# Kernel optimization log

Hardware: AMD Instinct MI355X
Metric: run time of the kernel (lower is better)

## Reference

```python
import jax, jax.numpy as jnp
import numpy as np

B, T, C = 4, 2048, 1024
NH = 16
HD = C // NH  # 64

def setup_inputs() -> dict:
    key = jax.random.key(0)
    k1, k2, k3 = jax.random.split(key, 3)
    x = jax.random.normal(k1, (B, T, C), dtype=jnp.float32)
    w_qkv = jax.random.normal(k2, (C, 3 * C), dtype=jnp.float32) * (1.0 / np.sqrt(C))
    w_out = jax.random.normal(k3, (C, C), dtype=jnp.float32) * (1.0 / np.sqrt(C))
    b_out = jnp.zeros((C,), dtype=jnp.float32)
    return {"x": x, "w_qkv": w_qkv, "w_out": w_out, "b_out": b_out}

def reference(x, w_qkv, w_out, b_out):
    b, t, c = x.shape
    nh, hd = NH, c // NH
    qkv = x @ w_qkv                      # [b, t, 3c]
    q, k, v = jnp.split(qkv, 3, axis=-1)
    # [b, t, c] -> [b, nh, t, hd]
    def heads(z):
        return z.reshape(b, t, nh, hd).transpose(0, 2, 1, 3)
    q, k, v = heads(q), heads(k), heads(v)
    scale = 1.0 / jnp.sqrt(jnp.asarray(hd, dtype=x.dtype))
    scores = jnp.einsum('bhqd,bhkd->bhqk', q, k) * scale  # [b, nh, t, t]
    causal = jnp.tril(jnp.ones((t, t), dtype=bool))
    scores = jnp.where(causal, scores, jnp.asarray(-jnp.inf, dtype=scores.dtype))
    attn = jax.nn.softmax(scores, axis=-1)
    ctx = jnp.einsum('bhqk,bhkd->bhqd', attn, v)           # [b, nh, t, hd]
    ctx = ctx.transpose(0, 2, 1, 3).reshape(b, t, c)
    return ctx @ w_out + b_out
```

## Files before the change

### kernel.cpp

```cpp
#include <hip/hip_runtime.h>
#include <cmath>


typedef __bf16 bf16x4 __attribute__((ext_vector_type(4)));
typedef __bf16 bf16x8 __attribute__((ext_vector_type(8)));
typedef float  f32x4  __attribute__((ext_vector_type(4)));
typedef float  f32x16 __attribute__((ext_vector_type(16)));

__device__ __forceinline__ void gload_lds16(const __bf16* g, __bf16* l) {
    __builtin_amdgcn_global_load_lds(
        (const __attribute__((address_space(1))) void*)g,
        (__attribute__((address_space(3))) void*)l,
        16, 0, 0);
}

__device__ __forceinline__ unsigned packbf(float a, float b) {
    union { __bf16 h[2]; unsigned u; } t;
    t.h[0] = (__bf16)a; t.h[1] = (__bf16)b;
    return t.u;
}

__device__ __forceinline__ void permswap(unsigned& a, unsigned& b) {
    asm volatile("v_permlane32_swap_b32 %0, %1" : "+v"(a), "+v"(b));
}

#define BAR()  __builtin_amdgcn_s_barrier()
#define VM2()  { asm volatile("s_waitcnt vmcnt(2)" ::: "memory"); \
                 __builtin_amdgcn_sched_barrier(0); }

__global__ __launch_bounds__(256) void cast_bf16(const float* __restrict__ in,
                                                 __bf16* __restrict__ out, int n4) {
    int i = blockIdx.x * 256 + threadIdx.x;
    if (i >= n4) return;
    float4 f = *(const float4*)(in + (size_t)i * 4);
    bf16x4 o;
    o[0] = (__bf16)f.x; o[1] = (__bf16)f.y; o[2] = (__bf16)f.z; o[3] = (__bf16)f.w;
    *(bf16x4*)(out + (size_t)i * 4) = o;
}

__global__ __launch_bounds__(256) void transpose_cast(const float* __restrict__ W,
                                                      __bf16* __restrict__ WT,
                                                      int K, int N) {
    __shared__ float tile[32][33];
    const int n0 = blockIdx.x * 32, k0 = blockIdx.y * 32;
    const int tx = threadIdx.x & 31, ty = threadIdx.x >> 5;
    #pragma unroll
    for (int i = 0; i < 4; ++i)
        tile[ty + 8 * i][tx] = W[(size_t)(k0 + ty + 8 * i) * N + n0 + tx];
    __syncthreads();
    #pragma unroll
    for (int i = 0; i < 4; ++i)
        WT[(size_t)(n0 + ty + 8 * i) * K + k0 + tx] = (__bf16)tile[tx][ty + 8 * i];
}

__global__ __launch_bounds__(256) void transpose_v(const __bf16* __restrict__ qkv,
                                                   __bf16* __restrict__ Vt) {
    constexpr int T = 2048, R3C = 3072;
    __shared__ __bf16 tile[64][72];
    const int bh = blockIdx.y;
    const int b  = bh >> 4, h = bh & 15;
    const int kt = blockIdx.x * 64;
    const int tid = threadIdx.x;
    #pragma unroll
    for (int i = 0; i < 2; ++i) {
        int idx = tid + 256 * i;
        int kr  = idx >> 3;
        int c8  = idx & 7;
        *(uint4*)&tile[kr][c8 * 8] =
            *(const uint4*)(qkv + (size_t)(b * T + kt + kr) * R3C + 2048 + h * 64 + c8 * 8);
    }
    __syncthreads();
    #pragma unroll
    for (int i = 0; i < 2; ++i) {
        int idx = tid + 256 * i;
        int d   = idx >> 3;
        int k8  = idx & 7;
        union { __bf16 v[8]; uint4 u; } t;
        #pragma unroll
        for (int j = 0; j < 8; ++j) t.v[j] = tile[k8 * 8 + j][d];
        *(uint4*)(Vt + ((size_t)bh * 64 + d) * T + kt + k8 * 8) = t.u;
    }
}

__global__ __launch_bounds__(512) void gemm256(const __bf16* __restrict__ A,
                                               const __bf16* __restrict__ BT,
                                               __bf16* __restrict__ Cc,
                                               int M, int N, int K) {
    __shared__ __attribute__((aligned(16))) char lds[131072];
    const int tid = threadIdx.x, lane = tid & 63, w = tid >> 6;
    const int wr = w >> 2, wc = w & 3, cc = lane & 15, gg = lane >> 4;

    const int cpx = gridDim.x >> 3;
    const int swz = ((int)blockIdx.x & 7) * cpx + ((int)blockIdx.x >> 3);
    const int nbx = N >> 8;
    const int rowBase = (swz / nbx) << 8;
    const int colBase = (swz % nbx) << 8;
    const int NT = K >> 6;

    const int sChunk = (lane & 7) ^ (((lane >> 5) & 1) << 1);
    const int rsub   = lane >> 3;

    auto stA = [&](int t, int h) {
        const int buf = t & 1, k0 = (t % NT) * 64;
        #pragma unroll
        for (int l = 0; l < 2; ++l) {
            int idx   = l * 8 + w;
            int rbase = ((idx >> 3) << 7) + h * 64 + ((idx & 7) << 3);
            gload_lds16(A + (size_t)(rowBase + rbase + rsub) * K + k0 + sChunk * 8,
                        (__bf16*)(lds + buf * 65536 + rbase * 128 + lane * 16));
        }
    };
    auto stB = [&](int t, int h) {
        const int buf = t & 1, k0 = (t % NT) * 64;
        #pragma unroll
        for (int l = 0; l < 2; ++l) {
            int idx   = l * 8 + w;
            int rbase = ((idx >> 2) << 6) + h * 32 + ((idx & 3) << 3);
            gload_lds16(BT + (size_t)(colBase + rbase + rsub) * K + k0 + sChunk * 8,
                        (__bf16*)(lds + buf * 65536 + 32768 + rbase * 128 + lane * 16));
        }
    };

    f32x4 acc[8][4];
    #pragma unroll
    for (int i = 0; i < 8; ++i)
        #pragma unroll
        for (int j = 0; j < 4; ++j) acc[i][j] = f32x4{0.f, 0.f, 0.f, 0.f};
    bf16x8 afr[8], bfr[8];

    auto rdA = [&](int buf, int mh) {
        const char* base = lds + buf * 65536;
        #pragma unroll
        for (int i = 0; i < 4; ++i)
            #pragma unroll
            for (int kk = 0; kk < 2; ++kk) {
                int r  = wr * 128 + mh * 64 + i * 16 + cc;
                int cb = (kk * 64 + gg * 16) ^ (((cc >> 2) & 1) << 5);
                afr[i * 2 + kk] = *(const bf16x8*)(base + r * 128 + cb);
            }
    };
    auto rdB = [&](int buf) {
        const char* base = lds + buf * 65536 + 32768;
        #pragma unroll
        for (int j = 0; j < 4; ++j)
            #pragma unroll
            for (int kk = 0; kk < 2; ++kk) {
                int r  = wc * 64 + j * 16 + cc;
                int cb = (kk * 64 + gg * 16) ^ (((cc >> 2) & 1) << 5);
                bfr[j * 2 + kk] = *(const bf16x8*)(base + r * 128 + cb);
            }
    };

#define QMFMA(MH, NH)                                                        \
    _Pragma("unroll") for (int i = 0; i < 4; ++i)                            \
    _Pragma("unroll") for (int j = 0; j < 2; ++j)                            \
    _Pragma("unroll") for (int kk = 0; kk < 2; ++kk)                         \
        acc[(MH)*4 + i][(NH)*2 + j] = __builtin_amdgcn_mfma_f32_16x16x32_bf16( \
            afr[i*2 + kk], bfr[((NH)*2 + j)*2 + kk], acc[(MH)*4 + i][(NH)*2 + j], 0, 0, 0);

    stA(0, 0); stB(0, 0); stA(0, 1); stB(0, 1); stA(1, 0);
    VM2(); BAR();

    for (int t = 0; t < NT; ++t) {
        const int buf = t & 1;
        rdA(buf, 0); rdB(buf);
        stB(t + 1, 0);
        BAR();
        __builtin_amdgcn_s_setprio(1); QMFMA(0, 0); __builtin_amdgcn_s_setprio(0);
        BAR();
        stA(t + 1, 1);
        BAR();
        __builtin_amdgcn_s_setprio(1); QMFMA(0, 1); __builtin_amdgcn_s_setprio(0);
        BAR();
        rdA(buf, 1);
        stB(t + 1, 1);
        BAR();
        __builtin_amdgcn_s_setprio(1); QMFMA(1, 0); __builtin_amdgcn_s_setprio(0);
        BAR();
        stA(t + 2, 0);
        BAR();
        __builtin_amdgcn_s_setprio(1); QMFMA(1, 1); __builtin_amdgcn_s_setprio(0);
        VM2(); BAR();
    }
#undef QMFMA

    #pragma unroll
    for (int i = 0; i < 8; ++i)
        #pragma unroll
        for (int j = 0; j < 4; ++j) {
            const int col = colBase + wc * 64 + j * 16 + cc;
            #pragma unroll
            for (int rr = 0; rr < 4; ++rr) {
                const int row = rowBase + wr * 128 + (i >> 2) * 64 + (i & 3) * 16 + gg * 4 + rr;
                Cc[(size_t)row * N + col] = (__bf16)acc[i][j][rr];
            }
        }
}

template <typename OutT, bool BIAS>
__global__ __launch_bounds__(256) void gemm_bt(const __bf16* __restrict__ A,
                                               const __bf16* __restrict__ BT,
                                               OutT* __restrict__ Cc,
                                               const float* __restrict__ bias,
                                               int M, int N, int K) {
    __shared__ __bf16 As[128 * 32];
    __shared__ __bf16 Bs[128 * 32];

    const int tid  = threadIdx.x;
    const int lane = tid & 63;
    const int w    = tid >> 6;
    const int wr   = w >> 1, wc = w & 1;
    const int cc   = lane & 15, gg = lane >> 4;
    const int rowBase = blockIdx.y * 128;
    const int colBase = blockIdx.x * 128;

    f32x4 acc[4][4];
    #pragma unroll
    for (int i = 0; i < 4; ++i)
        #pragma unroll
        for (int j = 0; j < 4; ++j) acc[i][j] = f32x4{0.f, 0.f, 0.f, 0.f};

    for (int k0 = 0; k0 < K; k0 += 32) {
        __syncthreads();
        #pragma unroll
        for (int i = 0; i < 2; ++i) {
            int idx = tid + 256 * i;
            int r   = idx >> 2;
            int c4  = idx & 3;
            gload_lds16(A  + (size_t)(rowBase + r) * K + k0 + c4 * 8, &As[idx * 8]);
            gload_lds16(BT + (size_t)(colBase + r) * K + k0 + c4 * 8, &Bs[idx * 8]);
        }
        __syncthreads();

        bf16x8 af[4], bfr2[4];
        #pragma unroll
        for (int i = 0; i < 4; ++i)
            af[i] = *(const bf16x8*)&As[(wr * 64 + i * 16 + cc) * 32 + gg * 8];
        #pragma unroll
        for (int j = 0; j < 4; ++j)
            bfr2[j] = *(const bf16x8*)&Bs[(wc * 64 + j * 16 + cc) * 32 + gg * 8];
        #pragma unroll
        for (int i = 0; i < 4; ++i)
            #pragma unroll
            for (int j = 0; j < 4; ++j)
                acc[i][j] = __builtin_amdgcn_mfma_f32_16x16x32_bf16(af[i], bfr2[j], acc[i][j], 0, 0, 0);
    }

    #pragma unroll
    for (int i = 0; i < 4; ++i)
        #pragma unroll
        for (int j = 0; j < 4; ++j) {
            const int col = colBase + wc * 64 + j * 16 + cc;
            #pragma unroll
            for (int r = 0; r < 4; ++r) {
                const int row = rowBase + wr * 64 + i * 16 + gg * 4 + r;
                float v = acc[i][j][r];
                if (BIAS) v += bias[col];
                Cc[(size_t)row * N + col] = (OutT)v;
            }
        }
}

__global__ __launch_bounds__(256) void flash_attn_mfma(const __bf16* __restrict__ qkv,
                                                       const __bf16* __restrict__ Vt,
                                                       __bf16* __restrict__ ctx) {
    constexpr int T = 2048, C = 1024, HD = 64;
    constexpr int R3C = 3 * C;
    constexpr float K1 = 0.125f * 1.44269504088896f;
    constexpr float K2 = -16.0f * 1.44269504088896f;

    const int tid  = threadIdx.x;
    const int lane = tid & 63;
    const int w    = tid >> 6;
    const int q5   = lane & 31;
    const int half = lane >> 5;

    const int bh   = blockIdx.x;
    const int y    = blockIdx.y;
    const int qtA  = 15 - y;
    const int qtB  = y;
    const int b    = bh >> 4;
    const int h    = bh & 15;
    const int srowA = qtA * 128 + w * 32;
    const int srowB = qtB * 128 + w * 32;
    const int ktmaxA = qtA * 128 + 64;
    const int ktmaxB = qtB * 128 + 64;

    __shared__ __attribute__((aligned(16))) __bf16 Ks [64][72];
    __shared__ __attribute__((aligned(16))) __bf16 VsT[64][72];

    const __bf16* QrowA = qkv + (size_t)(b * T + srowA + q5) * R3C + h * HD;
    const __bf16* QrowB = qkv + (size_t)(b * T + srowB + q5) * R3C + h * HD;
    bf16x8 QbA[4], QbB[4];
    #pragma unroll
    for (int ks = 0; ks < 4; ++ks) {
        QbA[ks] = *(const bf16x8*)(QrowA + ks * 16 + half * 8);
        QbB[ks] = *(const bf16x8*)(QrowB + ks * 16 + half * 8);
    }

    f32x16 OA[2], OB[2];
    #pragma unroll
    for (int mb = 0; mb < 2; ++mb)
        #pragma unroll
        for (int r = 0; r < 16; ++r) { OA[mb][r] = 0.f; OB[mb][r] = 0.f; }
    float lsumA = 0.f, lsumB = 0.f;

    const __bf16* Kb  = qkv + (size_t)(b * T) * R3C + C + h * HD;
    const __bf16* Vtb = Vt + (size_t)bh * 64 * T;

    for (int kt = 0; kt <= ktmaxA; kt += 64) {
        __syncthreads();
        #pragma unroll
        for (int i = 0; i < 2; ++i) {
            int idx = tid + 256 * i;
            int kr  = idx >> 3;
            int c8  = idx & 7;
            *(uint4*)&Ks[kr][c8 * 8] = *(const uint4*)(Kb + (size_t)(kt + kr) * R3C + c8 * 8);
        }
        #pragma unroll
        for (int i = 0; i < 2; ++i) {
            int idx = tid + 256 * i;
            int d   = idx >> 3;
            int k8  = idx & 7;
            *(uint4*)&VsT[d][k8 * 8] = *(const uint4*)(Vtb + (size_t)d * T + kt + k8 * 8);
        }
        __syncthreads();

        auto subtile = [&](int sub, const bf16x8* Qb, int srow, f32x16* O, float& lsum) {
            f32x16 S;
            #pragma unroll
            for (int r = 0; r < 16; ++r) S[r] = 0.f;
            #pragma unroll
            for (int ks = 0; ks < 4; ++ks) {
                bf16x8 kb = *(const bf16x8*)&Ks[sub * 32 + q5][ks * 16 + half * 8];
                S = __builtin_amdgcn_mfma_f32_32x32x16_bf16(kb, Qb[ks], S, 0, 0, 0);
            }
            if (kt + sub * 32 + 31 > srow) {
                #pragma unroll
                for (int r = 0; r < 16; ++r) {
                    int key = kt + sub * 32 + (r & 3) + 8 * (r >> 2) + 4 * half;
                    if (key > srow + q5) S[r] = -1e30f;
                }
            }
            float p[16];
            #pragma unroll
            for (int r = 0; r < 16; ++r) {
                p[r] = exp2f(fmaf(S[r], K1, K2));
                lsum += p[r];
            }
            unsigned w0 = packbf(p[0],  p[1]);
            unsigned w1 = packbf(p[2],  p[3]);
            unsigned w2 = packbf(p[4],  p[5]);
            unsigned w3 = packbf(p[6],  p[7]);
            permswap(w0, w2);
            permswap(w1, w3);
            unsigned w4 = packbf(p[8],  p[9]);
            unsigned w5 = packbf(p[10], p[11]);
            unsigned w6 = packbf(p[12], p[13]);
            unsigned w7 = packbf(p[14], p[15]);
            permswap(w4, w6);
            permswap(w5, w7);
            union { unsigned u[4]; bf16x8 v; } pf0, pf1;
            pf0.u[0] = w0; pf0.u[1] = w1; pf0.u[2] = w2; pf0.u[3] = w3;
            pf1.u[0] = w4; pf1.u[1] = w5; pf1.u[2] = w6; pf1.u[3] = w7;
            const int vc = sub * 32 + half * 8;
            #pragma unroll
            for (int mb = 0; mb < 2; ++mb) {
                bf16x8 v0 = *(const bf16x8*)&VsT[mb * 32 + q5][vc];
                O[mb] = __builtin_amdgcn_mfma_f32_32x32x16_bf16(v0, pf0.v, O[mb], 0, 0, 0);
                bf16x8 v1 = *(const bf16x8*)&VsT[mb * 32 + q5][vc + 16];
                O[mb] = __builtin_amdgcn_mfma_f32_32x32x16_bf16(v1, pf1.v, O[mb], 0, 0, 0);
            }
        };

        #pragma unroll
        for (int sub = 0; sub < 2; ++sub)
            subtile(sub, QbA, srowA, OA, lsumA);
        if (kt <= ktmaxB) {
            #pragma unroll
            for (int sub = 0; sub < 2; ++sub)
                subtile(sub, QbB, srowB, OB, lsumB);
        }
    }

    const float invA = 1.f / (lsumA + __shfl_xor(lsumA, 32));
    const float invB = 1.f / (lsumB + __shfl_xor(lsumB, 32));

    __bf16* crowA = ctx + (size_t)(b * T + srowA + q5) * C + h * HD;
    __bf16* crowB = ctx + (size_t)(b * T + srowB + q5) * C + h * HD;
    #pragma unroll
    for (int mb = 0; mb < 2; ++mb)
        #pragma unroll
        for (int a = 0; a < 4; ++a) {
            union { bf16x4 v; uint2 u; } pA, pB;
            #pragma unroll
            for (int bq = 0; bq < 4; ++bq) {
                pA.v[bq] = (__bf16)(OA[mb][4 * a + bq] * invA);
                pB.v[bq] = (__bf16)(OB[mb][4 * a + bq] * invB);
            }
            *(uint2*)(crowA + mb * 32 + 8 * a + 4 * half) = pA.u;
            *(uint2*)(crowB + mb * 32 + 8 * a + 4 * half) = pB.u;
        }
}

extern "C" void kernel_launch(void* const* d_in, const int* in_sizes, int n_in,
                              void* d_out, int out_size, void* d_ws, size_t ws_size,
                              hipStream_t stream) {
    constexpr int B = 4, T = 2048, C = 1024;
    constexpr int M = B * T;

    const float* x     = (const float*)d_in[0];
    const float* w_qkv = (const float*)d_in[1];
    const float* w_out = (const float*)d_in[2];
    const float* b_out = (const float*)d_in[3];
    float* out = (float*)d_out;

    char* ws = (char*)d_ws;
    __bf16* xb     = (__bf16*)(ws);
    __bf16* wqkvT  = (__bf16*)(ws + (16ull << 20));
    __bf16* woutT  = (__bf16*)(ws + (22ull << 20));
    __bf16* qkvb   = (__bf16*)(ws + (24ull << 20));
    __bf16* ctxb   = (__bf16*)(ws + (72ull << 20));
    __bf16* Vt     = (__bf16*)(ws + (88ull << 20));

    cast_bf16<<<(M * C / 4 + 255) / 256, 256, 0, stream>>>(x, xb, M * C / 4);
    transpose_cast<<<dim3(3 * C / 32, C / 32), 256, 0, stream>>>(w_qkv, wqkvT, C, 3 * C);
    transpose_cast<<<dim3(C / 32, C / 32), 256, 0, stream>>>(w_out, woutT, C, C);

    gemm256<<<384, 512, 0, stream>>>(xb, wqkvT, qkvb, M, 3 * C, C);

    transpose_v<<<dim3(T / 64, B * 16), 256, 0, stream>>>(qkvb, Vt);

    flash_attn_mfma<<<dim3(B * 16, 8), 256, 0, stream>>>(qkvb, Vt, ctxb);

    gemm_bt<float, true><<<dim3(C / 128, M / 128), 256, 0, stream>>>(
        ctxb, woutT, out, b_out, M, C, C);
}
```

Before: 289.1 us.

## Double-buffer K/V tiles with async global-to-LDS loads and XOR swizzle

Replaces the synchronous register-staged K and V^T tile loads in the attention kernel with direct global-to-LDS loads into two ping-pong buffers. The next tile is prefetched while the current one is consumed, and the per-iteration barriers drop from two to one. The padded LDS rows are replaced by an XOR swizzle on the 16-byte chunk index, applied on the global side, to avoid bank conflicts. This doubles LDS usage and relies on correct wait counts before the barrier for the async loads.

```diff
diff --git a/kernel.cpp b/kernel.cpp
--- a/kernel.cpp
+++ b/kernel.cpp
@@ -286,8 +286,8 @@
     const int ktmaxA = qtA * 128 + 64;
     const int ktmaxB = qtB * 128 + 64;
 
-    __shared__ __attribute__((aligned(16))) __bf16 Ks [64][72];
-    __shared__ __attribute__((aligned(16))) __bf16 VsT[64][72];
+    __shared__ __attribute__((aligned(16))) __bf16 KsL[2][64][64];
+    __shared__ __attribute__((aligned(16))) __bf16 VsL[2][64][64];
 
     const __bf16* QrowA = qkv + (size_t)(b * T + srowA + q5) * R3C + h * HD;
     const __bf16* QrowB = qkv + (size_t)(b * T + srowB + q5) * R3C + h * HD;
@@ -308,31 +308,47 @@
     const __bf16* Kb  = qkv + (size_t)(b * T) * R3C + C + h * HD;
     const __bf16* Vtb = Vt + (size_t)bh * 64 * T;
 
-    for (int kt = 0; kt <= ktmaxA; kt += 64) {
-        __syncthreads();
+    auto stage = [&](int bufi, int kt) {
         #pragma unroll
         for (int i = 0; i < 2; ++i) {
             int idx = tid + 256 * i;
             int kr  = idx >> 3;
             int c8  = idx & 7;
-            *(uint4*)&Ks[kr][c8 * 8] = *(const uint4*)(Kb + (size_t)(kt + kr) * R3C + c8 * 8);
+            int cs  = c8 ^ (kr & 7);
+            gload_lds16(Kb + (size_t)(kt + kr) * R3C + cs * 8,
+                        &KsL[bufi][kr][c8 * 8]);
         }
         #pragma unroll
         for (int i = 0; i < 2; ++i) {
             int idx = tid + 256 * i;
             int d   = idx >> 3;
             int k8  = idx & 7;
-            *(uint4*)&VsT[d][k8 * 8] = *(const uint4*)(Vtb + (size_t)d * T + kt + k8 * 8);
-        }
-        __syncthreads();
+            int ks_ = k8 ^ (d & 7);
+            gload_lds16(Vtb + (size_t)d * T + kt + ks_ * 8,
+                        &VsL[bufi][d][k8 * 8]);
+        }
+    };
+
+    stage(0, 0);
+    __syncthreads();
+
+    for (int kt = 0; kt <= ktmaxA; kt += 64) {
+        const int cur = (kt >> 6) & 1;
+        if (kt + 64 <= ktmaxA) stage(cur ^ 1, kt + 64);
+
+        const char* kbase = (const char*)KsL[cur];
+        const char* vbase = (const char*)VsL[cur];
 
         auto subtile = [&](int sub, const bf16x8* Qb, int srow, f32x16* O, float& lsum) {
             f32x16 S;
             #pragma unroll
             for (int r = 0; r < 16; ++r) S[r] = 0.f;
+            const int krow = sub * 32 + q5;
+            const int kxor = (krow & 7) << 4;
             #pragma unroll
             for (int ks = 0; ks < 4; ++ks) {
-                bf16x8 kb = *(const bf16x8*)&Ks[sub * 32 + q5][ks * 16 + half * 8];
+                bf16x8 kb = *(const bf16x8*)(kbase + krow * 128 +
+                                             (((ks * 16 + half * 8) * 2) ^ kxor));
                 S = __builtin_amdgcn_mfma_f32_32x32x16_bf16(kb, Qb[ks], S, 0, 0, 0);
             }
             if (kt + sub * 32 + 31 > srow) {
@@ -366,9 +382,11 @@
             const int vc = sub * 32 + half * 8;
             #pragma unroll
             for (int mb = 0; mb < 2; ++mb) {
-                bf16x8 v0 = *(const bf16x8*)&VsT[mb * 32 + q5][vc];
+                const int vrow = mb * 32 + q5;
+                const int vxor = (vrow & 7) << 4;
+                bf16x8 v0 = *(const bf16x8*)(vbase + vrow * 128 + ((vc * 2) ^ vxor));
                 O[mb] = __builtin_amdgcn_mfma_f32_32x32x16_bf16(v0, pf0.v, O[mb], 0, 0, 0);
-                bf16x8 v1 = *(const bf16x8*)&VsT[mb * 32 + q5][vc + 16];
+                bf16x8 v1 = *(const bf16x8*)(vbase + vrow * 128 + (((vc + 16) * 2) ^ vxor));
                 O[mb] = __builtin_amdgcn_mfma_f32_32x32x16_bf16(v1, pf1.v, O[mb], 0, 0, 0);
             }
         };
@@ -381,6 +399,8 @@
             for (int sub = 0; sub < 2; ++sub)
                 subtile(sub, QbB, srowB, OB, lsumB);
         }
+
+        __syncthreads();
     }
 
     const float invA = 1.f / (lsumA + __shfl_xor(lsumA, 32));
```

Measured after the change: 294.8 us. Within noise of the previous version (+2.0%).
